# Performance work log

Measured on AMD Instinct MI355X. Metric: run time of the kernel, lower is better.

The kernel has to match this reference:

```python
import jax, jax.numpy as jnp
import numpy as np

DIM = 2048
H = 16        # num query heads
KVH = 4       # num kv heads
HD = DIM // H # head_dim = 128
RD = 64       # rope_dims (< head_dim -> partial rope)
BASE = 10000.0
SCALE = HD ** -0.5
EPS_RMS = 1e-6
EPS_NORM = 1e-12


def _rms_norm(x):
    return x * jax.lax.rsqrt(jnp.mean(x * x, axis=-1, keepdims=True) + EPS_RMS)


def _rope_cache(T):
    inv_freq = 1.0 / (BASE ** (jnp.arange(0, RD, 2, dtype=jnp.float32) / RD))  # [RD/2]
    t = jnp.arange(T, dtype=jnp.float32)
    freqs = t[:, None] * inv_freq[None, :]  # [T, RD/2]
    return jnp.cos(freqs)[None, None], jnp.sin(freqs)[None, None]  # [1,1,T,RD/2]


def _apply_rope(x, cos, sin):
    # x: [B, H, T, HD]; rotate first RD dims, pass through the rest
    x_rope, x_pass = x[..., :RD], x[..., RD:]
    half = RD // 2
    x1, x2 = x_rope[..., :half], x_rope[..., half:]
    x_rot = jnp.concatenate([x1 * cos - x2 * sin, x2 * cos + x1 * sin], axis=-1)
    return jnp.concatenate([x_rot, x_pass], axis=-1)


def setup_inputs() -> dict:
    key = jax.random.key(0)
    ks = jax.random.split(key, 6)
    x = jax.random.normal(ks[0], (4, 2048, DIM), dtype=jnp.float32)
    Wq = jax.random.normal(ks[1], (DIM, DIM), dtype=jnp.float32) * 0.02
    Wk = jax.random.normal(ks[2], (KVH * HD, DIM), dtype=jnp.float32) * 0.02
    Wv = jax.random.normal(ks[3], (KVH * HD, DIM), dtype=jnp.float32) * 0.02
    Wproj = jax.random.normal(ks[4], (DIM, DIM), dtype=jnp.float32) * 0.02
    q_gain = jnp.ones((H,), dtype=jnp.float32)
    return {"x": x, "Wq": Wq, "Wk": Wk, "Wv": Wv, "Wproj": Wproj, "q_gain": q_gain}


def reference(x, Wq, Wk, Wv, Wproj, q_gain):
    B, T, _ = x.shape
    # projections (nn.Linear: x @ W.T)  ->  [B, heads, T, HD]
    q = (x @ Wq.T).reshape(B, T, H, HD).transpose(0, 2, 1, 3)
    k = (x @ Wk.T).reshape(B, T, KVH, HD).transpose(0, 2, 1, 3)
    v = (x @ Wv.T).reshape(B, T, KVH, HD).transpose(0, 2, 1, 3)

    cos, sin = _rope_cache(T)
    q = _apply_rope(_rms_norm(q), cos, sin) * q_gain[None, :, None, None]
    k = _apply_rope(_rms_norm(k), cos, sin)

    # GQA: expand kv heads (kv head i serves query heads i*rep .. i*rep+rep-1)
    rep = H // KVH
    k = jnp.repeat(k, rep, axis=1)      # [B, H, T, HD]
    v_attn = jnp.repeat(v, rep, axis=1)  # [B, H, T, HD]

    # causal SDPA
    scores = jnp.einsum("bhqd,bhkd->bhqk", q, k) * SCALE
    causal = jnp.tril(jnp.ones((T, T), dtype=bool))
    scores = jnp.where(causal[None, None], scores, jnp.finfo(scores.dtype).min)
    attn = jax.nn.softmax(scores, axis=-1)
    y = jnp.einsum("bhqk,bhkd->bhqd", attn, v_attn)

    # xsa postproc: remove component of y along unit value direction
    vn = v_attn / jnp.maximum(
        jnp.linalg.norm(v_attn, axis=-1, keepdims=True), EPS_NORM)
    y = y - jnp.sum(y * vn, axis=-1, keepdims=True) * vn

    y = y.transpose(0, 2, 1, 3).reshape(B, T, DIM)
    return y @ Wproj.T
```

## Files before the change

kernel.cpp:

```cpp
#include <hip/hip_runtime.h>
#include <cstdint>
#include <cstddef>

typedef __bf16 bf16_t;
typedef __bf16 bf16x4 __attribute__((ext_vector_type(4)));
typedef __bf16 bf16x8 __attribute__((ext_vector_type(8)));
typedef float f32x4 __attribute__((ext_vector_type(4)));

#define B_ 4
#define T_ 2048
#define DIM_ 2048
#define H_ 16
#define KVH_ 4
#define HD_ 128
#define QKV_ 3072
#define QSCALE (0.08838834764831845f * 1.4426950408889634f)

__device__ __forceinline__ void gload16(const bf16_t* g, bf16_t* l) {
  __builtin_amdgcn_global_load_lds(
      (const __attribute__((address_space(1))) unsigned int*)g,
      (__attribute__((address_space(3))) unsigned int*)l, 16, 0, 0);
}

__global__ __launch_bounds__(256) void cvt_all(const float4* __restrict__ x,
                                               const float4* __restrict__ wq,
                                               const float4* __restrict__ wk,
                                               const float4* __restrict__ wv,
                                               const float4* __restrict__ wp,
                                               bf16x4* __restrict__ xb,
                                               bf16x4* __restrict__ wqkvb,
                                               bf16x4* __restrict__ wpb) {
  int i = blockIdx.x * 256 + threadIdx.x;
  const float4* s;
  bf16x4* dst;
  int off;
  if (i < 4194304) { s = x; dst = xb; off = i; }
  else if (i < 5242880) { s = wq; dst = wqkvb; off = i - 4194304; }
  else if (i < 5505024) { s = wk; dst = wqkvb + 1048576; off = i - 5242880; }
  else if (i < 5767168) { s = wv; dst = wqkvb + 1310720; off = i - 5505024; }
  else { s = wp; dst = wpb; off = i - 5767168; }
  float4 v = s[off];
  bf16x4 o = {(__bf16)v.x, (__bf16)v.y, (__bf16)v.z, (__bf16)v.w};
  dst[off] = o;
}

#define STAGE2(gsrc, ldst, KK)                                  \
  do {                                                          \
    gload16((gsrc), (ldst) + tid * 8);                          \
    gload16((gsrc) + (size_t)128 * (KK), (ldst) + 4096 + tid * 8); \
  } while (0)

__global__ __launch_bounds__(512, 2) void gemm_bt(const bf16_t* __restrict__ A,
                                                  const bf16_t* __restrict__ B,
                                                  void* __restrict__ Cp,
                                                  int M, int N, int K, int out_bf16) {
  __shared__ __align__(16) bf16_t Ab[2 * 16384];
  __shared__ __align__(16) bf16_t Bb[2 * 16384];
  const int tid = threadIdx.x;
  const int w = tid >> 6, lane = tid & 63;
  const int m16 = lane & 15, q4 = lane >> 4;
  const int wr = w >> 2, wc = w & 3;
  const int rowBase = blockIdx.y * 256, colBase = blockIdx.x * 256;

  const int srow = tid >> 2, skc = tid & 3;
  const int sswz = (skc ^ (srow & 3) ^ ((srow >> 2) & 3)) & 3;
  const bf16_t* srcA = A + (size_t)(rowBase + srow) * K + sswz * 8;
  const bf16_t* srcB = B + (size_t)(colBase + srow) * K + sswz * 8;

  const int cs = (q4 ^ (m16 & 3) ^ ((m16 >> 2) & 3)) & 3;
  const int aoff = wr * 4096 + m16 * 32 + cs * 8;
  const int boff = wc * 2048 + m16 * 32 + cs * 8;

  f32x4 acc[8][4];
#pragma unroll
  for (int i = 0; i < 8; ++i)
#pragma unroll
    for (int j = 0; j < 4; ++j) acc[i][j] = (f32x4){0.f, 0.f, 0.f, 0.f};

  const int nt = K >> 6;
  STAGE2(srcA, Ab, K);
  STAGE2(srcB, Bb, K);
  STAGE2(srcA + 32, Ab + 8192, K);
  STAGE2(srcB + 32, Bb + 8192, K);
  asm volatile("s_waitcnt vmcnt(4)" ::: "memory");
  __builtin_amdgcn_s_barrier();

#pragma unroll 1
  for (int t = 0; t < nt; ++t) {
    const int cb = (t & 1) << 14, nb = cb ^ 16384;
    const int pk = ((t + 1 < nt) ? t + 1 : t) << 6;
    const bf16_t* Ac = Ab + cb + aoff;
    const bf16_t* Bc = Bb + cb + boff;
    bf16x8 a[4], b[4];

    STAGE2(srcA + pk, Ab + nb, K);
#pragma unroll
    for (int i = 0; i < 4; ++i) a[i] = *(const bf16x8*)(Ac + i * 512);
#pragma unroll
    for (int j = 0; j < 4; ++j) b[j] = *(const bf16x8*)(Bc + j * 512);
    __builtin_amdgcn_s_barrier();
    asm volatile("s_waitcnt lgkmcnt(0)" ::: "memory");
    __builtin_amdgcn_sched_barrier(0);
    __builtin_amdgcn_s_setprio(1);
#pragma unroll
    for (int i = 0; i < 4; ++i)
#pragma unroll
      for (int j = 0; j < 4; ++j)
        acc[i][j] = __builtin_amdgcn_mfma_f32_16x16x32_bf16(a[i], b[j], acc[i][j], 0, 0, 0);
    __builtin_amdgcn_s_setprio(0);
    __builtin_amdgcn_s_barrier();

    STAGE2(srcB + pk, Bb + nb, K);
#pragma unroll
    for (int i = 0; i < 4; ++i) a[i] = *(const bf16x8*)(Ac + (4 + i) * 512);
    __builtin_amdgcn_s_barrier();
    asm volatile("s_waitcnt lgkmcnt(0)" ::: "memory");
    __builtin_amdgcn_sched_barrier(0);
    __builtin_amdgcn_s_setprio(1);
#pragma unroll
    for (int i = 0; i < 4; ++i)
#pragma unroll
      for (int j = 0; j < 4; ++j)
        acc[4 + i][j] = __builtin_amdgcn_mfma_f32_16x16x32_bf16(a[i], b[j], acc[4 + i][j], 0, 0, 0);
    __builtin_amdgcn_s_setprio(0);
    asm volatile("s_waitcnt vmcnt(4)" ::: "memory");
    __builtin_amdgcn_s_barrier();

    STAGE2(srcA + pk + 32, Ab + nb + 8192, K);
#pragma unroll
    for (int i = 0; i < 4; ++i) a[i] = *(const bf16x8*)(Ac + 8192 + i * 512);
#pragma unroll
    for (int j = 0; j < 4; ++j) b[j] = *(const bf16x8*)(Bc + 8192 + j * 512);
    __builtin_amdgcn_s_barrier();
    asm volatile("s_waitcnt lgkmcnt(0)" ::: "memory");
    __builtin_amdgcn_sched_barrier(0);
    __builtin_amdgcn_s_setprio(1);
#pragma unroll
    for (int i = 0; i < 4; ++i)
#pragma unroll
      for (int j = 0; j < 4; ++j)
        acc[i][j] = __builtin_amdgcn_mfma_f32_16x16x32_bf16(a[i], b[j], acc[i][j], 0, 0, 0);
    __builtin_amdgcn_s_setprio(0);
    __builtin_amdgcn_s_barrier();

    STAGE2(srcB + pk + 32, Bb + nb + 8192, K);
#pragma unroll
    for (int i = 0; i < 4; ++i) a[i] = *(const bf16x8*)(Ac + 8192 + (4 + i) * 512);
    __builtin_amdgcn_s_barrier();
    asm volatile("s_waitcnt lgkmcnt(0)" ::: "memory");
    __builtin_amdgcn_sched_barrier(0);
    __builtin_amdgcn_s_setprio(1);
#pragma unroll
    for (int i = 0; i < 4; ++i)
#pragma unroll
      for (int j = 0; j < 4; ++j)
        acc[4 + i][j] = __builtin_amdgcn_mfma_f32_16x16x32_bf16(a[i], b[j], acc[4 + i][j], 0, 0, 0);
    __builtin_amdgcn_s_setprio(0);
    asm volatile("s_waitcnt vmcnt(4)" ::: "memory");
    __builtin_amdgcn_s_barrier();
  }

  if (out_bf16) {
    bf16_t* C = (bf16_t*)Cp;
#pragma unroll
    for (int i = 0; i < 8; ++i)
#pragma unroll
      for (int j = 0; j < 4; ++j)
#pragma unroll
        for (int r = 0; r < 4; ++r) {
          int row = rowBase + wr * 128 + i * 16 + q4 * 4 + r;
          int col = colBase + wc * 64 + j * 16 + m16;
          C[(size_t)row * N + col] = (bf16_t)acc[i][j][r];
        }
  } else {
    float* C = (float*)Cp;
#pragma unroll
    for (int i = 0; i < 8; ++i)
#pragma unroll
      for (int j = 0; j < 4; ++j)
#pragma unroll
        for (int r = 0; r < 4; ++r) {
          int row = rowBase + wr * 128 + i * 16 + q4 * 4 + r;
          int col = colBase + wc * 64 + j * 16 + m16;
          C[(size_t)row * N + col] = acc[i][j][r];
        }
  }
}

__global__ __launch_bounds__(256) void gemm_qkv(const bf16_t* __restrict__ A,
                                                const bf16_t* __restrict__ Bw,
                                                bf16_t* __restrict__ qkv,
                                                bf16_t* __restrict__ vt,
                                                const float* __restrict__ gain) {
  __shared__ bf16_t As[2 * 128 * 32];
  __shared__ bf16_t Bs[2 * 128 * 32];
  __shared__ float ssbuf[2][128];
  const int tid = threadIdx.x;
  const int w = tid >> 6, lane = tid & 63;
  const int m = lane & 15, quad = lane >> 4;
  const int wr = w >> 1, wc = w & 1;
  const int rowBase = blockIdx.y * 128, colBase = blockIdx.x * 128;

  f32x4 acc[4][4];
#pragma unroll
  for (int i = 0; i < 4; ++i)
#pragma unroll
    for (int j = 0; j < 4; ++j) acc[i][j] = (f32x4){0.f, 0.f, 0.f, 0.f};

  for (int t = 0; t < 32; ++t) {
    const int k0 = t << 6;
#pragma unroll
    for (int i2 = 0; i2 < 4; ++i2) {
      int idx = i2 * 256 + tid;
      int half = idx >> 9, row = (idx >> 2) & 127, kc = idx & 3;
      int gk = k0 + half * 32 + kc * 8;
      gload16(A + (size_t)(rowBase + row) * 2048 + gk, &As[idx * 8]);
      gload16(Bw + (size_t)(colBase + row) * 2048 + gk, &Bs[idx * 8]);
    }
    asm volatile("s_waitcnt vmcnt(4)" ::: "memory");
    __builtin_amdgcn_s_barrier();
    {
      bf16x8 a[4], bb[4];
#pragma unroll
      for (int i = 0; i < 4; ++i)
        a[i] = *(const bf16x8*)&As[(wr * 64 + i * 16 + m) * 32 + quad * 8];
#pragma unroll
      for (int j = 0; j < 4; ++j)
        bb[j] = *(const bf16x8*)&Bs[(wc * 64 + j * 16 + m) * 32 + quad * 8];
#pragma unroll
      for (int i = 0; i < 4; ++i)
#pragma unroll
        for (int j = 0; j < 4; ++j)
          acc[i][j] = __builtin_amdgcn_mfma_f32_16x16x32_bf16(a[i], bb[j], acc[i][j], 0, 0, 0);
    }
    asm volatile("s_waitcnt vmcnt(0)" ::: "memory");
    __builtin_amdgcn_s_barrier();
    {
      const bf16_t* Ah = As + 4096;
      const bf16_t* Bh = Bs + 4096;
      bf16x8 a[4], bb[4];
#pragma unroll
      for (int i = 0; i < 4; ++i)
        a[i] = *(const bf16x8*)&Ah[(wr * 64 + i * 16 + m) * 32 + quad * 8];
#pragma unroll
      for (int j = 0; j < 4; ++j)
        bb[j] = *(const bf16x8*)&Bh[(wc * 64 + j * 16 + m) * 32 + quad * 8];
#pragma unroll
      for (int i = 0; i < 4; ++i)
#pragma unroll
        for (int j = 0; j < 4; ++j)
          acc[i][j] = __builtin_amdgcn_mfma_f32_16x16x32_bf16(a[i], bb[j], acc[i][j], 0, 0, 0);
    }
    __syncthreads();
  }

  const int bx = blockIdx.x;
  if (bx < 20) {
    const float g = (bx < 16) ? gain[bx] * QSCALE : 1.0f;
#pragma unroll
    for (int i = 0; i < 4; ++i) {
      float ssp[4];
#pragma unroll
      for (int r = 0; r < 4; ++r) {
        float s = 0.f;
#pragma unroll
        for (int j = 0; j < 4; ++j) s += acc[i][j][r] * acc[i][j][r];
#pragma unroll
        for (int off = 1; off <= 8; off <<= 1) s += __shfl_xor(s, off);
        ssp[r] = s;
      }
      if (m == 0) {
#pragma unroll
        for (int r = 0; r < 4; ++r) ssbuf[wc][wr * 64 + i * 16 + quad * 4 + r] = ssp[r];
      }
    }
    __syncthreads();
    const float if0 = exp2f(-(float)m * 0.4152410118609203f);
    const float if1 = exp2f(-(float)(16 + m) * 0.4152410118609203f);
#pragma unroll
    for (int i = 0; i < 4; ++i) {
#pragma unroll
      for (int r = 0; r < 4; ++r) {
        const int ridx = wr * 64 + i * 16 + quad * 4 + r;
        const int row = rowBase + ridx;
        const float rn = rsqrtf((ssbuf[0][ridx] + ssbuf[1][ridx]) * (1.f / 128.f) + 1e-6f);
        float v0 = acc[i][0][r] * rn, v1 = acc[i][1][r] * rn;
        float v2 = acc[i][2][r] * rn, v3 = acc[i][3][r] * rn;
        float o0 = v0, o1 = v1, o2 = v2, o3 = v3;
        if (wc == 0) {
          const float t2 = (float)(row & (T_ - 1));
          const float a0 = t2 * if0, a1 = t2 * if1;
          const float c0_ = cosf(a0), s0_ = sinf(a0);
          const float c1_ = cosf(a1), s1_ = sinf(a1);
          o0 = v0 * c0_ - v2 * s0_;
          o1 = v1 * c1_ - v3 * s1_;
          o2 = v2 * c0_ + v0 * s0_;
          o3 = v3 * c1_ + v1 * s1_;
        }
        bf16_t* out = qkv + (size_t)row * QKV_ + colBase + wc * 64 + m;
        out[0]  = (bf16_t)(o0 * g);
        out[16] = (bf16_t)(o1 * g);
        out[32] = (bf16_t)(o2 * g);
        out[48] = (bf16_t)(o3 * g);
      }
    }
  } else {
    const int kvh = bx - 20;
#pragma unroll
    for (int i = 0; i < 4; ++i)
#pragma unroll
      for (int j = 0; j < 4; ++j) {
        const int row0 = rowBase + wr * 64 + i * 16 + quad * 4;
        const int d = wc * 64 + j * 16 + m;
        bf16x4 pv;
#pragma unroll
        for (int r = 0; r < 4; ++r) {
          pv[r] = (bf16_t)acc[i][j][r];
          qkv[(size_t)(row0 + r) * QKV_ + colBase + d] = pv[r];
        }
        const int b = row0 >> 11, t0 = row0 & (T_ - 1);
        *(bf16x4*)(vt + ((size_t)(b * KVH_ + kvh) * HD_ + d) * T_ + t0) = pv;
      }
  }
}

__global__ __launch_bounds__(256) void attn_kernel(const bf16_t* __restrict__ qkv,
                                                   const bf16_t* __restrict__ vt,
                                                   bf16_t* __restrict__ y) {
  __shared__ __align__(16) bf16_t Ks[2][64 * 128];
  __shared__ __align__(16) bf16_t Vs[2][128 * 64];
  __shared__ __align__(16) bf16_t Ps[4][32 * 40];

  const int tid = threadIdx.x;
  const int w = tid >> 6, lane = tid & 63;
  const int m = lane & 15, q = lane >> 4;
  const int h = blockIdx.y, b = blockIdx.z, kvh = h >> 2;

  const bf16_t* qptr = qkv + (size_t)(b * T_) * QKV_ + h * HD_;
  const bf16_t* kptr = qkv + (size_t)(b * T_) * QKV_ + DIM_ + kvh * HD_;
  const bf16_t* vptr = qkv + (size_t)(b * T_) * QKV_ + DIM_ + KVH_ * HD_ + kvh * HD_;
  const bf16_t* vtptr = vt + (size_t)(b * KVH_ + kvh) * HD_ * T_;

  const int kKeyR = tid >> 4;
  const int kSrcO = (((tid & 15) ^ kKeyR) & 15) * 8;
  const int vDR = tid >> 3;
  const int vSrcO = (((tid & 7) ^ (vDR & 7)) & 7) * 8;

  int koff[2][4], vbase[8], poff[2], vslot8[2];
#pragma unroll
  for (int kf = 0; kf < 2; ++kf)
#pragma unroll
    for (int c = 0; c < 4; ++c)
      koff[kf][c] = (kf * 16 + m) * 128 + (((c * 4 + q) ^ m) & 15) * 8;
#pragma unroll
  for (int f = 0; f < 8; ++f) vbase[f] = (f * 16 + m) * 64;
  vslot8[0] = ((q ^ (m & 7)) & 7) * 8;
  vslot8[1] = (((4 + q) ^ (m & 7)) & 7) * 8;
#pragma unroll
  for (int qf = 0; qf < 2; ++qf) poff[qf] = (qf * 16 + m) * 40 + q * 8;

#define ATTN_STAGE(buf, kb0)                                                  \
  do {                                                                        \
    _Pragma("unroll")                                                         \
    for (int i2 = 0; i2 < 4; ++i2)                                            \
      gload16(kptr + (size_t)((kb0) + i2 * 16 + kKeyR) * QKV_ + kSrcO,        \
              &Ks[buf][(i2 * 256 + tid) * 8]);                                \
    _Pragma("unroll")                                                         \
    for (int i2 = 0; i2 < 4; ++i2)                                            \
      gload16(vtptr + (size_t)(i2 * 32 + vDR) * T_ + (kb0) + vSrcO,           \
              &Vs[buf][(i2 * 256 + tid) * 8]);                                \
  } while (0)

#pragma unroll 1
  for (int ti = 0; ti < 2; ++ti) {
    const int qb = ((ti == 0) ? (15 - (int)blockIdx.x) : (int)blockIdx.x) * 128;
    const int qbw = qb + w * 32;
    const int nk = (qb >> 6) + 2;

    bf16x8 aq[2][4];
#pragma unroll
    for (int qf = 0; qf < 2; ++qf)
#pragma unroll
      for (int c = 0; c < 4; ++c)
        aq[qf][c] = *(const bf16x8*)(qptr + (size_t)(qbw + qf * 16 + m) * QKV_ + c * 32 + q * 8);

    f32x4 o[2][8];
#pragma unroll
    for (int qf = 0; qf < 2; ++qf)
#pragma unroll
      for (int f = 0; f < 8; ++f) o[qf][f] = (f32x4){0.f, 0.f, 0.f, 0.f};
    float l_r[2] = {0.f, 0.f};

    ATTN_STAGE(0, 0);

#pragma unroll 1
    for (int it = 0; it < nk; ++it) {
      const int kb = it << 6;
      __syncthreads();

      if (it + 1 < nk) ATTN_STAGE((it + 1) & 1, kb + 64);

#pragma unroll
      for (int s = 0; s < 2; ++s) {
        const int kbs = kb + s * 32;
        if (kbs > qbw + 31) continue;
        const bf16_t* Kb = &Ks[it & 1][s * 4096];
        const bf16_t* Vb = Vs[it & 1];

        f32x4 S[2][2];
#pragma unroll
        for (int qf = 0; qf < 2; ++qf)
#pragma unroll
          for (int kf = 0; kf < 2; ++kf) S[qf][kf] = (f32x4){0.f, 0.f, 0.f, 0.f};
#pragma unroll
        for (int kf = 0; kf < 2; ++kf)
#pragma unroll
          for (int c = 0; c < 4; ++c) {
            bf16x8 ak = *(const bf16x8*)&Kb[koff[kf][c]];
            S[0][kf] = __builtin_amdgcn_mfma_f32_16x16x32_bf16(ak, aq[0][c], S[0][kf], 0, 0, 0);
            S[1][kf] = __builtin_amdgcn_mfma_f32_16x16x32_bf16(ak, aq[1][c], S[1][kf], 0, 0, 0);
          }

        const bool needmask = (kbs + 31) > qbw;
#pragma unroll
        for (int qf = 0; qf < 2; ++qf) {
          const int qrow = qbw + qf * 16 + m;
          if (needmask) {
#pragma unroll
            for (int kf = 0; kf < 2; ++kf)
#pragma unroll
              for (int r = 0; r < 4; ++r) {
                int key = kbs + kf * 16 + q * 4 + r;
                if (key > qrow) S[qf][kf][r] = -1e30f;
              }
          }
          float rs = 0.f;
#pragma unroll
          for (int kf = 0; kf < 2; ++kf)
#pragma unroll
            for (int r = 0; r < 4; ++r) {
              float p = exp2f(S[qf][kf][r]);
              S[qf][kf][r] = p;
              rs += p;
            }
          l_r[qf] += rs;
#pragma unroll
          for (int kf = 0; kf < 2; ++kf) {
            bf16x4 pk = {(__bf16)S[qf][kf][0], (__bf16)S[qf][kf][1],
                         (__bf16)S[qf][kf][2], (__bf16)S[qf][kf][3]};
            *(bf16x4*)&Ps[w][(qf * 16 + m) * 40 + kf * 16 + q * 4] = pk;
          }
        }
        asm volatile("s_waitcnt lgkmcnt(0)" ::: "memory");

        bf16x8 Pb[2];
#pragma unroll
        for (int qf = 0; qf < 2; ++qf)
          Pb[qf] = *(const bf16x8*)&Ps[w][poff[qf]];
#pragma unroll
        for (int f = 0; f < 8; ++f) {
          bf16x8 av = *(const bf16x8*)&Vb[vbase[f] + vslot8[s]];
          o[0][f] = __builtin_amdgcn_mfma_f32_16x16x32_bf16(av, Pb[0], o[0][f], 0, 0, 0);
          o[1][f] = __builtin_amdgcn_mfma_f32_16x16x32_bf16(av, Pb[1], o[1][f], 0, 0, 0);
        }
      }
    }

#pragma unroll
    for (int qf = 0; qf < 2; ++qf) {
      const int trow = qbw + qf * 16 + m;
      float lt = l_r[qf];
      lt += __shfl_xor(lt, 16);
      lt += __shfl_xor(lt, 32);
      const float linv = 1.f / lt;
      bf16x4 vv[8];
      float n2 = 0.f, dp = 0.f;
#pragma unroll
      for (int f = 0; f < 8; ++f) {
        vv[f] = *(const bf16x4*)(vptr + (size_t)trow * QKV_ + f * 16 + q * 4);
#pragma unroll
        for (int r = 0; r < 4; ++r) {
          float v = (float)vv[f][r];
          n2 += v * v;
          dp += o[qf][f][r] * linv * v;
        }
      }
      n2 += __shfl_xor(n2, 16); n2 += __shfl_xor(n2, 32);
      dp += __shfl_xor(dp, 16); dp += __shfl_xor(dp, 32);
      float d = fmaxf(sqrtf(n2), 1e-12f);
      float coef = dp / (d * d);
#pragma unroll
      for (int f = 0; f < 8; ++f) {
        bf16x4 yo;
#pragma unroll
        for (int r = 0; r < 4; ++r)
          yo[r] = (bf16_t)(o[qf][f][r] * linv - coef * (float)vv[f][r]);
        *(bf16x4*)(y + (size_t)(b * T_ + trow) * DIM_ + h * HD_ + f * 16 + q * 4) = yo;
      }
    }
    __syncthreads();
  }
}

extern "C" void kernel_launch(void* const* d_in, const int* in_sizes, int n_in,
                              void* d_out, int out_size, void* d_ws, size_t ws_size,
                              hipStream_t stream) {
  const float* x = (const float*)d_in[0];
  const float* Wq = (const float*)d_in[1];
  const float* Wk = (const float*)d_in[2];
  const float* Wv = (const float*)d_in[3];
  const float* Wp = (const float*)d_in[4];
  const float* qg = (const float*)d_in[5];

  bf16_t* xbf = (bf16_t*)d_ws;
  bf16_t* wqkv = xbf + (size_t)8192 * 2048;
  bf16_t* wproj = wqkv + (size_t)3072 * 2048;
  bf16_t* qkv = wproj + (size_t)2048 * 2048;
  bf16_t* vt = qkv + (size_t)8192 * 3072;
  bf16_t* ybf = xbf;

  cvt_all<<<26624, 256, 0, stream>>>((const float4*)x, (const float4*)Wq,
                                     (const float4*)Wk, (const float4*)Wv,
                                     (const float4*)Wp, (bf16x4*)xbf,
                                     (bf16x4*)wqkv, (bf16x4*)wproj);
  gemm_qkv<<<dim3(24, 64), 256, 0, stream>>>(xbf, wqkv, qkv, vt, qg);
  attn_kernel<<<dim3(8, 16, 4), 256, 0, stream>>>(qkv, vt, ybf);
  gemm_bt<<<dim3(8, 32), 512, 0, stream>>>(ybf, wproj, d_out, 8192, 2048, 2048, 0);
}
```

Baseline: 497.1 us.

## Triple-buffer QKV GEMM LDS tiles with two-stage-ahead async prefetch

Replaces the QKV projection GEMM's per-iteration load-then-compute structure with a 3-slot LDS ring. Loads for k-step s+2 are issued while step s is computed, and there is one barrier per 32-wide k-step instead of a full __syncthreads drain per 64-wide step. The goal is to hide global-to-LDS latency behind MFMA work. It costs 50% more shared memory, and the clamped tail reloads redundant data.

```diff
diff --git a/kernel.cpp b/kernel.cpp
--- a/kernel.cpp
+++ b/kernel.cpp
@@ -187,13 +187,26 @@
   }
 }
 
+#define QKV_ISSUE(ss, rr)                                                     \
+  do {                                                                        \
+    const int gk_ = (ss) << 5;                                                \
+    bf16_t* Ad_ = As + (rr) * 4096;                                           \
+    bf16_t* Bd_ = Bs + (rr) * 4096;                                           \
+    gload16(A + (size_t)(rowBase + r0) * 2048 + gk_ + c0 * 8, Ad_ + tid * 8); \
+    gload16(Bw + (size_t)(colBase + r0) * 2048 + gk_ + c0 * 8, Bd_ + tid * 8);\
+    gload16(A + (size_t)(rowBase + r1) * 2048 + gk_ + c0 * 8,                 \
+            Ad_ + (256 + tid) * 8);                                           \
+    gload16(Bw + (size_t)(colBase + r1) * 2048 + gk_ + c0 * 8,                \
+            Bd_ + (256 + tid) * 8);                                           \
+  } while (0)
+
 __global__ __launch_bounds__(256) void gemm_qkv(const bf16_t* __restrict__ A,
                                                 const bf16_t* __restrict__ Bw,
                                                 bf16_t* __restrict__ qkv,
                                                 bf16_t* __restrict__ vt,
                                                 const float* __restrict__ gain) {
-  __shared__ bf16_t As[2 * 128 * 32];
-  __shared__ bf16_t Bs[2 * 128 * 32];
+  __shared__ bf16_t As[3 * 128 * 32];
+  __shared__ bf16_t Bs[3 * 128 * 32];
   __shared__ float ssbuf[2][128];
   const int tid = threadIdx.x;
   const int w = tid >> 6, lane = tid & 63;
@@ -201,57 +214,43 @@
   const int wr = w >> 1, wc = w & 1;
   const int rowBase = blockIdx.y * 128, colBase = blockIdx.x * 128;
 
+  const int r0 = tid >> 2, c0 = tid & 3;
+  const int r1 = (256 + tid) >> 2;
+
   f32x4 acc[4][4];
 #pragma unroll
   for (int i = 0; i < 4; ++i)
 #pragma unroll
     for (int j = 0; j < 4; ++j) acc[i][j] = (f32x4){0.f, 0.f, 0.f, 0.f};
 
-  for (int t = 0; t < 32; ++t) {
-    const int k0 = t << 6;
-#pragma unroll
-    for (int i2 = 0; i2 < 4; ++i2) {
-      int idx = i2 * 256 + tid;
-      int half = idx >> 9, row = (idx >> 2) & 127, kc = idx & 3;
-      int gk = k0 + half * 32 + kc * 8;
-      gload16(A + (size_t)(rowBase + row) * 2048 + gk, &As[idx * 8]);
-      gload16(Bw + (size_t)(colBase + row) * 2048 + gk, &Bs[idx * 8]);
+  QKV_ISSUE(0, 0);
+  QKV_ISSUE(1, 1);
+
+  int rc = 0, ri = 2;
+#pragma unroll 1
+  for (int s = 0; s < 64; ++s) {
+    asm volatile("s_waitcnt vmcnt(4)" ::: "memory");
+    __builtin_amdgcn_s_barrier();
+    {
+      const int s2 = (s + 2 < 64) ? s + 2 : 63;
+      QKV_ISSUE(s2, ri);
     }
-    asm volatile("s_waitcnt vmcnt(4)" ::: "memory");
-    __builtin_amdgcn_s_barrier();
-    {
-      bf16x8 a[4], bb[4];
-#pragma unroll
-      for (int i = 0; i < 4; ++i)
-        a[i] = *(const bf16x8*)&As[(wr * 64 + i * 16 + m) * 32 + quad * 8];
-#pragma unroll
-      for (int j = 0; j < 4; ++j)
-        bb[j] = *(const bf16x8*)&Bs[(wc * 64 + j * 16 + m) * 32 + quad * 8];
-#pragma unroll
-      for (int i = 0; i < 4; ++i)
-#pragma unroll
-        for (int j = 0; j < 4; ++j)
-          acc[i][j] = __builtin_amdgcn_mfma_f32_16x16x32_bf16(a[i], bb[j], acc[i][j], 0, 0, 0);
-    }
-    asm volatile("s_waitcnt vmcnt(0)" ::: "memory");
-    __builtin_amdgcn_s_barrier();
-    {
-      const bf16_t* Ah = As + 4096;
-      const bf16_t* Bh = Bs + 4096;
-      bf16x8 a[4], bb[4];
-#pragma unroll
-      for (int i = 0; i < 4; ++i)
-        a[i] = *(const bf16x8*)&Ah[(wr * 64 + i * 16 + m) * 32 + quad * 8];
-#pragma unroll
-      for (int j = 0; j < 4; ++j)
-        bb[j] = *(const bf16x8*)&Bh[(wc * 64 + j * 16 + m) * 32 + quad * 8];
-#pragma unroll
-      for (int i = 0; i < 4; ++i)
-#pragma unroll
-        for (int j = 0; j < 4; ++j)
-          acc[i][j] = __builtin_amdgcn_mfma_f32_16x16x32_bf16(a[i], bb[j], acc[i][j], 0, 0, 0);
-    }
-    __syncthreads();
+    const bf16_t* Ah = As + rc * 4096;
+    const bf16_t* Bh = Bs + rc * 4096;
+    bf16x8 a[4], bb[4];
+#pragma unroll
+    for (int i = 0; i < 4; ++i)
+      a[i] = *(const bf16x8*)&Ah[(wr * 64 + i * 16 + m) * 32 + quad * 8];
+#pragma unroll
+    for (int j = 0; j < 4; ++j)
+      bb[j] = *(const bf16x8*)&Bh[(wc * 64 + j * 16 + m) * 32 + quad * 8];
+#pragma unroll
+    for (int i = 0; i < 4; ++i)
+#pragma unroll
+      for (int j = 0; j < 4; ++j)
+        acc[i][j] = __builtin_amdgcn_mfma_f32_16x16x32_bf16(a[i], bb[j], acc[i][j], 0, 0, 0);
+    rc = (rc == 2) ? 0 : rc + 1;
+    ri = (ri == 2) ? 0 : ri + 1;
   }
 
   const int bx = blockIdx.x;
```

New measurement: 556.6 us. +12.0%, slower.
